# Optimization experiments

Measured on AMD Instinct MI355X. Metric: run time of the kernel, lower is better.

## Reference

```python
import jax, jax.numpy as jnp
import numpy as np

NUM_HEADS = 16
THETA = 10000.0


def _rope(x, pos):
    # x: [B, H, S, d_k], pos: [S] int. Rotate consecutive pairs (even, odd).
    d = x.shape[-1]
    inv_freq = THETA ** (-jnp.arange(0, d, 2, dtype=jnp.float32) / d)  # [d/2]
    ang = pos.astype(jnp.float32)[:, None] * inv_freq                  # [S, d/2]
    cos, sin = jnp.cos(ang), jnp.sin(ang)
    x1, x2 = x[..., 0::2], x[..., 1::2]
    out = jnp.stack([x1 * cos - x2 * sin, x1 * sin + x2 * cos], axis=-1)
    return out.reshape(x.shape)


def setup_inputs() -> dict:
    key = jax.random.key(0)
    k1, k2, k3 = jax.random.split(key, 3)
    B, S, D = 2, 2048, 1024
    x = jax.random.normal(k1, (B, S, D), dtype=jnp.float32)
    # scale weights like a trained init so attention logits are well-behaved
    W_qkv = jax.random.normal(k2, (3 * D, D), dtype=jnp.float32) * 0.02
    W_out = jax.random.normal(k3, (D, D), dtype=jnp.float32) * 0.02
    return {"x": x, "W_qkv": W_qkv, "W_out": W_out}


def reference(x, W_qkv, W_out):
    B, S, D = x.shape
    H = NUM_HEADS
    dk = D // H

    qkv = x @ W_qkv.T                                   # [B, S, 3D]
    q, k, v = jnp.split(qkv, 3, axis=-1)

    def to_heads(t):
        return t.reshape(B, S, H, dk).transpose(0, 2, 1, 3)  # [B, H, S, dk]

    q, k, v = to_heads(q), to_heads(k), to_heads(v)

    pos = jnp.arange(S)
    q = _rope(q, pos)
    k = _rope(k, pos)

    scale = 1.0 / jnp.sqrt(jnp.asarray(dk, dtype=x.dtype))
    logits = jnp.einsum('bhqd,bhkd->bhqk', q, k) * scale  # [B, H, S, S]
    causal = jnp.tril(jnp.ones((S, S), dtype=bool))
    logits = jnp.where(causal, logits, -jnp.inf)
    attn = jax.nn.softmax(logits, axis=-1)
    heads = jnp.einsum('bhqk,bhkd->bhqd', attn, v)        # [B, H, S, dk]
    merged = heads.transpose(0, 2, 1, 3).reshape(B, S, D)
    return merged @ W_out.T
```

## Files before the change

kernel.cpp:

```cpp
#include <hip/hip_runtime.h>
#include <hip/hip_bf16.h>
#include <math.h>

#define BATCH   2
#define SEQ     2048
#define DMODEL  1024
#define NHEAD   16
#define DK      64
#define MTOK    (BATCH*SEQ)
#define QKVN    (3*DMODEL)
#define BH      (BATCH*NHEAD)

typedef __attribute__((ext_vector_type(8))) __bf16 bf16x8;
typedef __attribute__((ext_vector_type(4))) float  f32x4;

#define GL16(gp, lp) __builtin_amdgcn_global_load_lds( \
    (const __attribute__((address_space(1))) unsigned int*)(gp), \
    (__attribute__((address_space(3))) unsigned int*)(lp), 16, 0, 0)

__global__ __launch_bounds__(256) void cvt_bf16(const float* __restrict__ in,
                                                __hip_bfloat16* __restrict__ out, int n) {
    int i = (blockIdx.x * 256 + threadIdx.x) * 4;
    if (i >= n) return;
    float4 v = *(const float4*)(in + i);
    __hip_bfloat162 a, b;
    a.x = __float2bfloat16(v.x); a.y = __float2bfloat16(v.y);
    b.x = __float2bfloat16(v.z); b.y = __float2bfloat16(v.w);
    *(__hip_bfloat162*)(out + i)     = a;
    *(__hip_bfloat162*)(out + i + 2) = b;
}

#define GBM 128
#define GBN 128
#define GBK 32

template<int OUT_BF16>
__global__ __launch_bounds__(256) void gemm_bf16_nt(const __hip_bfloat16* __restrict__ A,
                                                    const __hip_bfloat16* __restrict__ B,
                                                    void* __restrict__ Cv,
                                                    int M, int N, int K) {
    __shared__ __align__(16) __hip_bfloat16 As[GBM][GBK];
    __shared__ __align__(16) __hip_bfloat16 Bs[GBN][GBK];
    const int tid  = threadIdx.x;
    const int wid  = tid >> 6;
    const int lane = tid & 63;
    const int fr   = lane & 15;
    const int fq   = lane >> 4;
    const int wm   = (wid >> 1) * 64;
    const int wn   = (wid & 1) * 64;
    const int m0   = blockIdx.y * GBM;
    const int n0   = blockIdx.x * GBN;

    f32x4 acc[4][4];
#pragma unroll
    for (int m = 0; m < 4; m++)
#pragma unroll
        for (int n = 0; n < 4; n++) acc[m][n] = (f32x4)0.f;

    const __hip_bfloat16* a0 = A + (size_t)(m0 + (tid >> 2)) * K + (tid & 3) * 8;
    const __hip_bfloat16* a1 = a0 + (size_t)64 * K;
    const __hip_bfloat16* b0 = B + (size_t)(n0 + (tid >> 2)) * K + (tid & 3) * 8;
    const __hip_bfloat16* b1 = b0 + (size_t)64 * K;
    __hip_bfloat16* asd0 = &As[0][0] + tid * 8;
    __hip_bfloat16* asd1 = asd0 + 2048;
    __hip_bfloat16* bsd0 = &Bs[0][0] + tid * 8;
    __hip_bfloat16* bsd1 = bsd0 + 2048;

    const __hip_bfloat16* ArP = &As[wm + fr][0] + fq * 8;
    const __hip_bfloat16* BrP = &Bs[wn + fr][0] + fq * 8;

    for (int k0 = 0; k0 < K; k0 += GBK) {
        GL16(a0 + k0, asd0);
        GL16(a1 + k0, asd1);
        GL16(b0 + k0, bsd0);
        GL16(b1 + k0, bsd1);
        __syncthreads();

        bf16x8 af[4], bfv[4];
#pragma unroll
        for (int m = 0; m < 4; m++) af[m]  = *(const bf16x8*)(ArP + m * 512);
#pragma unroll
        for (int n = 0; n < 4; n++) bfv[n] = *(const bf16x8*)(BrP + n * 512);
#pragma unroll
        for (int m = 0; m < 4; m++)
#pragma unroll
            for (int n = 0; n < 4; n++)
                acc[m][n] = __builtin_amdgcn_mfma_f32_16x16x32_bf16(af[m], bfv[n], acc[m][n], 0, 0, 0);
        __syncthreads();
    }

#pragma unroll
    for (int m = 0; m < 4; m++)
#pragma unroll
        for (int n = 0; n < 4; n++)
#pragma unroll
            for (int r = 0; r < 4; r++) {
                size_t row = m0 + wm + m * 16 + fq * 4 + r;
                size_t col = n0 + wn + n * 16 + fr;
                if (OUT_BF16)
                    ((__hip_bfloat16*)Cv)[row * N + col] = __float2bfloat16(acc[m][n][r]);
                else
                    ((float*)Cv)[row * N + col] = acc[m][n][r];
            }
}

__global__ __launch_bounds__(256) void rope_qk(const __hip_bfloat16* __restrict__ qkvb,
                                               __hip_bfloat16* __restrict__ qh,
                                               __hip_bfloat16* __restrict__ kh) {
    int idx  = blockIdx.x * 256 + threadIdx.x;
    int row  = idx >> 10;
    int p    = idx & 1023;
    int half = p >> 9;
    int pp   = p & 511;
    int hh   = pp >> 5;
    int j    = pp & 31;
    int b    = row >> 11, s = row & (SEQ - 1);
    const __hip_bfloat16* src = qkvb + (size_t)row * QKVN + half * DMODEL + hh * DK + 2 * j;
    __hip_bfloat162 xv = *(const __hip_bfloat162*)src;
    float x1 = __bfloat162float(xv.x);
    float x2 = __bfloat162float(xv.y);
    float inv = exp2f(-(float)j * 0.41524101186092030f);
    float ang = (float)s * inv;
    float sn, cs;
    sincosf(ang, &sn, &cs);
    __hip_bfloat162 o;
    o.x = __float2bfloat16(x1 * cs - x2 * sn);
    o.y = __float2bfloat16(x1 * sn + x2 * cs);
    __hip_bfloat16* dst = (half ? kh : qh) + ((size_t)(b * NHEAD + hh) * SEQ + s) * DK + 2 * j;
    *(__hip_bfloat162*)dst = o;
}

__global__ __launch_bounds__(256) void v_trans(const __hip_bfloat16* __restrict__ qkvb,
                                               __hip_bfloat16* __restrict__ vt) {
    const int t  = threadIdx.x;
    const int s  = blockIdx.x * 256 + t;
    const int bh = blockIdx.y;
    const int b  = bh >> 4, h = bh & 15;
    const __hip_bfloat16* src = qkvb + (size_t)(b * SEQ + s) * QKVN + 2 * DMODEL + h * DK;
    __hip_bfloat16* dst = vt + (size_t)bh * DK * SEQ + s;
#pragma unroll
    for (int d2 = 0; d2 < 32; d2++) {
        __hip_bfloat162 v = *(const __hip_bfloat162*)(src + 2 * d2);
        dst[(size_t)(2 * d2) * SEQ]     = v.x;
        dst[(size_t)(2 * d2 + 1) * SEQ] = v.y;
    }
}

__global__ __launch_bounds__(256) void attn_mfma(const __hip_bfloat16* __restrict__ qh,
                                                 const __hip_bfloat16* __restrict__ kh,
                                                 const __hip_bfloat16* __restrict__ vt,
                                                 __hip_bfloat16* __restrict__ mergedb) {
    __shared__ __align__(16) __hip_bfloat16 Ps[4][2048];
    const int tid = threadIdx.x, wid = tid >> 6, lane = tid & 63;
    const int fr = lane & 15, fq = lane >> 4;
    const int bid = blockIdx.x;
    const int qt  = 15 - (bid >> 5);
    const int bh  = bid & 31;
    const int b   = bh >> 4, h = bh & 15;

    const size_t hoff = (size_t)bh * SEQ * DK;
    const __hip_bfloat16* Qb = qh + hoff;
    const __hip_bfloat16* Kb = kh + hoff;
    const __hip_bfloat16* Vb = vt + hoff;

    const int q0 = qt * 128 + wid * 32;

    bf16x8 qf[2][2];
#pragma unroll
    for (int m = 0; m < 2; m++)
#pragma unroll
        for (int c = 0; c < 2; c++)
            qf[m][c] = *(const bf16x8*)&Qb[(size_t)(q0 + m * 16 + fr) * DK + c * 32 + fq * 8];

    f32x4 o[2][4];
#pragma unroll
    for (int m = 0; m < 2; m++)
#pragma unroll
        for (int n = 0; n < 4; n++) o[m][n] = (f32x4)0.f;
    float mrun[8], lrun[8];
#pragma unroll
    for (int i = 0; i < 8; i++) { mrun[i] = -INFINITY; lrun[i] = 0.f; }

    char* Pw = (char*)&Ps[wid][0];
    const int nkt = 2 * qt + 2;

    for (int kt = 0; kt < nkt; kt++) {
        const int key0 = kt * 64;
        f32x4 s_acc[2][4];
#pragma unroll
        for (int m = 0; m < 2; m++)
#pragma unroll
            for (int n = 0; n < 4; n++) s_acc[m][n] = (f32x4)0.f;
#pragma unroll
        for (int n = 0; n < 4; n++) {
            bf16x8 k0f = *(const bf16x8*)&Kb[(size_t)(key0 + n * 16 + fr) * DK + fq * 8];
            bf16x8 k1f = *(const bf16x8*)&Kb[(size_t)(key0 + n * 16 + fr) * DK + 32 + fq * 8];
#pragma unroll
            for (int m = 0; m < 2; m++) {
                s_acc[m][n] = __builtin_amdgcn_mfma_f32_16x16x32_bf16(qf[m][0], k0f, s_acc[m][n], 0, 0, 0);
                s_acc[m][n] = __builtin_amdgcn_mfma_f32_16x16x32_bf16(qf[m][1], k1f, s_acc[m][n], 0, 0, 0);
            }
        }
#pragma unroll
        for (int m = 0; m < 2; m++)
#pragma unroll
            for (int n = 0; n < 4; n++)
#pragma unroll
                for (int r = 0; r < 4; r++) s_acc[m][n][r] *= 0.125f;
        if (kt >= 2 * qt) {
#pragma unroll
            for (int m = 0; m < 2; m++)
#pragma unroll
                for (int n = 0; n < 4; n++)
#pragma unroll
                    for (int r = 0; r < 4; r++) {
                        int qrow = q0 + m * 16 + fq * 4 + r;
                        int key  = key0 + n * 16 + fr;
                        if (key > qrow) s_acc[m][n][r] = -INFINITY;
                    }
        }
#pragma unroll
        for (int m = 0; m < 2; m++)
#pragma unroll
            for (int r = 0; r < 4; r++) {
                float mx = fmaxf(fmaxf(s_acc[m][0][r], s_acc[m][1][r]),
                                 fmaxf(s_acc[m][2][r], s_acc[m][3][r]));
                mx = fmaxf(mx, __shfl_xor(mx, 1));
                mx = fmaxf(mx, __shfl_xor(mx, 2));
                mx = fmaxf(mx, __shfl_xor(mx, 4));
                mx = fmaxf(mx, __shfl_xor(mx, 8));
                const int ri = m * 4 + r;
                float mnew = fmaxf(mrun[ri], mx);
                float corr = __expf(mrun[ri] - mnew);
                mrun[ri] = mnew;
                float rs = 0.f;
#pragma unroll
                for (int n = 0; n < 4; n++) {
                    float pv = __expf(s_acc[m][n][r] - mnew);
                    s_acc[m][n][r] = pv;
                    rs += pv;
                }
                rs += __shfl_xor(rs, 1);
                rs += __shfl_xor(rs, 2);
                rs += __shfl_xor(rs, 4);
                rs += __shfl_xor(rs, 8);
                lrun[ri] = lrun[ri] * corr + rs;
#pragma unroll
                for (int n = 0; n < 4; n++) o[m][n][r] *= corr;
            }
#pragma unroll
        for (int m = 0; m < 2; m++)
#pragma unroll
            for (int r = 0; r < 4; r++) {
                int rl = m * 16 + fq * 4 + r;
                int sw = (rl & 7) << 4;
#pragma unroll
                for (int n = 0; n < 4; n++) {
                    int key = n * 16 + fr;
                    *(__hip_bfloat16*)(Pw + (((rl << 7) + (key << 1)) ^ sw)) =
                        __float2bfloat16(s_acc[m][n][r]);
                }
            }
        asm volatile("s_waitcnt lgkmcnt(0)" ::: "memory");
        __builtin_amdgcn_sched_barrier(0);
        bf16x8 pa[2][2];
#pragma unroll
        for (int m = 0; m < 2; m++)
#pragma unroll
            for (int c = 0; c < 2; c++) {
                int rl = m * 16 + fr;
                pa[m][c] = *(const bf16x8*)(Pw + (((rl << 7) + ((c * 32 + fq * 8) << 1)) ^ ((rl & 7) << 4)));
            }
#pragma unroll
        for (int n = 0; n < 4; n++) {
            bf16x8 v0f = *(const bf16x8*)&Vb[(size_t)(n * 16 + fr) * SEQ + key0 + fq * 8];
            bf16x8 v1f = *(const bf16x8*)&Vb[(size_t)(n * 16 + fr) * SEQ + key0 + 32 + fq * 8];
#pragma unroll
            for (int m = 0; m < 2; m++) {
                o[m][n] = __builtin_amdgcn_mfma_f32_16x16x32_bf16(pa[m][0], v0f, o[m][n], 0, 0, 0);
                o[m][n] = __builtin_amdgcn_mfma_f32_16x16x32_bf16(pa[m][1], v1f, o[m][n], 0, 0, 0);
            }
        }
    }

#pragma unroll
    for (int m = 0; m < 2; m++)
#pragma unroll
        for (int r = 0; r < 4; r++) {
            float invl = 1.0f / lrun[m * 4 + r];
            int qrow = q0 + m * 16 + fq * 4 + r;
#pragma unroll
            for (int n = 0; n < 4; n++) {
                int col = h * DK + n * 16 + fr;
                mergedb[(size_t)(b * SEQ + qrow) * DMODEL + col] =
                    __float2bfloat16(o[m][n][r] * invl);
            }
        }
}

extern "C" void kernel_launch(void* const* d_in, const int* in_sizes, int n_in,
                              void* d_out, int out_size, void* d_ws, size_t ws_size,
                              hipStream_t stream) {
    const float* x    = (const float*)d_in[0];
    const float* Wqkv = (const float*)d_in[1];
    const float* Wout = (const float*)d_in[2];
    float* out = (float*)d_out;

    char* w = (char*)d_ws;
    __hip_bfloat16* qkvb   = (__hip_bfloat16*)(w);
    __hip_bfloat16* qh     = (__hip_bfloat16*)(w + (24u << 20));
    __hip_bfloat16* kh     = (__hip_bfloat16*)(w + (32u << 20));
    __hip_bfloat16* vt     = (__hip_bfloat16*)(w + (40u << 20));
    __hip_bfloat16* xb     = (__hip_bfloat16*)(w + (48u << 20));
    __hip_bfloat16* merged = (__hip_bfloat16*)(w + (48u << 20));
    __hip_bfloat16* wqkvb  = (__hip_bfloat16*)(w + (56u << 20));
    __hip_bfloat16* woutb  = (__hip_bfloat16*)(w + (62u << 20));

    cvt_bf16<<<MTOK * DMODEL / 1024, 256, 0, stream>>>(x, xb, MTOK * DMODEL);
    cvt_bf16<<<QKVN * DMODEL / 1024, 256, 0, stream>>>(Wqkv, wqkvb, QKVN * DMODEL);
    cvt_bf16<<<DMODEL * DMODEL / 1024, 256, 0, stream>>>(Wout, woutb, DMODEL * DMODEL);

    dim3 g1(QKVN / GBN, MTOK / GBM);
    gemm_bf16_nt<1><<<g1, 256, 0, stream>>>(xb, wqkvb, qkvb, MTOK, QKVN, DMODEL);

    rope_qk<<<MTOK * 1024 / 256, 256, 0, stream>>>(qkvb, qh, kh);
    v_trans<<<dim3(SEQ / 256, BH), 256, 0, stream>>>(qkvb, vt);

    attn_mfma<<<512, 256, 0, stream>>>(qh, kh, vt, merged);

    dim3 g3(DMODEL / GBN, MTOK / GBM);
    gemm_bf16_nt<0><<<g3, 256, 0, stream>>>(merged, woutb, out, MTOK, DMODEL, DMODEL);
}
```

Before: 263.0 us.

## Halve attention query tile, double grid, and transpose V through shared memory

```diff
diff --git a/kernel.cpp b/kernel.cpp
--- a/kernel.cpp
+++ b/kernel.cpp
@@ -132,17 +132,29 @@
 
 __global__ __launch_bounds__(256) void v_trans(const __hip_bfloat16* __restrict__ qkvb,
                                                __hip_bfloat16* __restrict__ vt) {
+    __shared__ __hip_bfloat16 Ts[64][72];
     const int t  = threadIdx.x;
-    const int s  = blockIdx.x * 256 + t;
+    const int s0 = blockIdx.x * 64;
     const int bh = blockIdx.y;
     const int b  = bh >> 4, h = bh & 15;
-    const __hip_bfloat16* src = qkvb + (size_t)(b * SEQ + s) * QKVN + 2 * DMODEL + h * DK;
-    __hip_bfloat16* dst = vt + (size_t)bh * DK * SEQ + s;
-#pragma unroll
-    for (int d2 = 0; d2 < 32; d2++) {
-        __hip_bfloat162 v = *(const __hip_bfloat162*)(src + 2 * d2);
-        dst[(size_t)(2 * d2) * SEQ]     = v.x;
-        dst[(size_t)(2 * d2 + 1) * SEQ] = v.y;
+    const int sl = t >> 3;
+    const int dc = (t & 7) * 8;
+#pragma unroll
+    for (int i = 0; i < 2; i++) {
+        int s = sl + i * 32;
+        bf16x8 v = *(const bf16x8*)&qkvb[(size_t)(b * SEQ + s0 + s) * QKVN + 2 * DMODEL + h * DK + dc];
+        *(bf16x8*)&Ts[s][dc] = v;
+    }
+    __syncthreads();
+    const int dl = t >> 3;
+    const int sc = (t & 7) * 8;
+#pragma unroll
+    for (int i = 0; i < 2; i++) {
+        int d = dl + i * 32;
+        bf16x8 o;
+#pragma unroll
+        for (int j = 0; j < 8; j++) o[j] = *(const __bf16*)&Ts[sc + j][d];
+        *(bf16x8*)&vt[(size_t)bh * DK * SEQ + (size_t)d * SEQ + s0 + sc] = o;
     }
 }
 
@@ -150,11 +162,11 @@
                                                  const __hip_bfloat16* __restrict__ kh,
                                                  const __hip_bfloat16* __restrict__ vt,
                                                  __hip_bfloat16* __restrict__ mergedb) {
-    __shared__ __align__(16) __hip_bfloat16 Ps[4][2048];
+    __shared__ __align__(16) __hip_bfloat16 Ps[4][1024];
     const int tid = threadIdx.x, wid = tid >> 6, lane = tid & 63;
     const int fr = lane & 15, fq = lane >> 4;
     const int bid = blockIdx.x;
-    const int qt  = 15 - (bid >> 5);
+    const int qt  = 31 - (bid >> 5);
     const int bh  = bid & 31;
     const int b   = bh >> 4, h = bh & 15;
 
@@ -163,139 +175,124 @@
     const __hip_bfloat16* Kb = kh + hoff;
     const __hip_bfloat16* Vb = vt + hoff;
 
-    const int q0 = qt * 128 + wid * 32;
-
-    bf16x8 qf[2][2];
-#pragma unroll
-    for (int m = 0; m < 2; m++)
-#pragma unroll
-        for (int c = 0; c < 2; c++)
-            qf[m][c] = *(const bf16x8*)&Qb[(size_t)(q0 + m * 16 + fr) * DK + c * 32 + fq * 8];
-
-    f32x4 o[2][4];
-#pragma unroll
-    for (int m = 0; m < 2; m++)
-#pragma unroll
-        for (int n = 0; n < 4; n++) o[m][n] = (f32x4)0.f;
-    float mrun[8], lrun[8];
-#pragma unroll
-    for (int i = 0; i < 8; i++) { mrun[i] = -INFINITY; lrun[i] = 0.f; }
+    const int q0 = qt * 64 + wid * 16;
+
+    bf16x8 qf[2];
+#pragma unroll
+    for (int c = 0; c < 2; c++)
+        qf[c] = *(const bf16x8*)&Qb[(size_t)(q0 + fr) * DK + c * 32 + fq * 8];
+
+    f32x4 o[4];
+#pragma unroll
+    for (int n = 0; n < 4; n++) o[n] = (f32x4)0.f;
+    float mrun[4], lrun[4];
+#pragma unroll
+    for (int i = 0; i < 4; i++) { mrun[i] = -INFINITY; lrun[i] = 0.f; }
 
     char* Pw = (char*)&Ps[wid][0];
-    const int nkt = 2 * qt + 2;
-
-    for (int kt = 0; kt < nkt; kt++) {
+
+    for (int kt = 0; kt <= qt; kt++) {
         const int key0 = kt * 64;
-        f32x4 s_acc[2][4];
-#pragma unroll
-        for (int m = 0; m < 2; m++)
-#pragma unroll
-            for (int n = 0; n < 4; n++) s_acc[m][n] = (f32x4)0.f;
+        bf16x8 kf[4][2];
+#pragma unroll
+        for (int n = 0; n < 4; n++)
+#pragma unroll
+            for (int c = 0; c < 2; c++)
+                kf[n][c] = *(const bf16x8*)&Kb[(size_t)(key0 + n * 16 + fr) * DK + c * 32 + fq * 8];
+        bf16x8 vf[4][2];
+#pragma unroll
+        for (int n = 0; n < 4; n++)
+#pragma unroll
+            for (int c = 0; c < 2; c++)
+                vf[n][c] = *(const bf16x8*)&Vb[(size_t)(n * 16 + fr) * SEQ + key0 + c * 32 + fq * 8];
+
+        f32x4 s_acc[4];
+#pragma unroll
+        for (int n = 0; n < 4; n++) s_acc[n] = (f32x4)0.f;
 #pragma unroll
         for (int n = 0; n < 4; n++) {
-            bf16x8 k0f = *(const bf16x8*)&Kb[(size_t)(key0 + n * 16 + fr) * DK + fq * 8];
-            bf16x8 k1f = *(const bf16x8*)&Kb[(size_t)(key0 + n * 16 + fr) * DK + 32 + fq * 8];
-#pragma unroll
-            for (int m = 0; m < 2; m++) {
-                s_acc[m][n] = __builtin_amdgcn_mfma_f32_16x16x32_bf16(qf[m][0], k0f, s_acc[m][n], 0, 0, 0);
-                s_acc[m][n] = __builtin_amdgcn_mfma_f32_16x16x32_bf16(qf[m][1], k1f, s_acc[m][n], 0, 0, 0);
+            s_acc[n] = __builtin_amdgcn_mfma_f32_16x16x32_bf16(qf[0], kf[n][0], s_acc[n], 0, 0, 0);
+            s_acc[n] = __builtin_amdgcn_mfma_f32_16x16x32_bf16(qf[1], kf[n][1], s_acc[n], 0, 0, 0);
+        }
+#pragma unroll
+        for (int n = 0; n < 4; n++)
+#pragma unroll
+            for (int r = 0; r < 4; r++) s_acc[n][r] *= 0.125f;
+        if (kt == qt) {
+#pragma unroll
+            for (int n = 0; n < 4; n++)
+#pragma unroll
+                for (int r = 0; r < 4; r++) {
+                    int qrow = q0 + fq * 4 + r;
+                    int key  = key0 + n * 16 + fr;
+                    if (key > qrow) s_acc[n][r] = -INFINITY;
+                }
+        }
+
+        float corr[4];
+#pragma unroll
+        for (int r = 0; r < 4; r++) {
+            float mx = fmaxf(fmaxf(s_acc[0][r], s_acc[1][r]),
+                             fmaxf(s_acc[2][r], s_acc[3][r]));
+            mx = fmaxf(mx, __shfl_xor(mx, 1));
+            mx = fmaxf(mx, __shfl_xor(mx, 2));
+            mx = fmaxf(mx, __shfl_xor(mx, 4));
+            mx = fmaxf(mx, __shfl_xor(mx, 8));
+            float mnew = fmaxf(mrun[r], mx);
+            corr[r] = __expf(mrun[r] - mnew);
+            mrun[r] = mnew;
+            float rs = 0.f;
+#pragma unroll
+            for (int n = 0; n < 4; n++) {
+                float pv = __expf(s_acc[n][r] - mnew);
+                s_acc[n][r] = pv;
+                rs += pv;
             }
-        }
-#pragma unroll
-        for (int m = 0; m < 2; m++)
-#pragma unroll
-            for (int n = 0; n < 4; n++)
-#pragma unroll
-                for (int r = 0; r < 4; r++) s_acc[m][n][r] *= 0.125f;
-        if (kt >= 2 * qt) {
-#pragma unroll
-            for (int m = 0; m < 2; m++)
-#pragma unroll
-                for (int n = 0; n < 4; n++)
-#pragma unroll
-                    for (int r = 0; r < 4; r++) {
-                        int qrow = q0 + m * 16 + fq * 4 + r;
-                        int key  = key0 + n * 16 + fr;
-                        if (key > qrow) s_acc[m][n][r] = -INFINITY;
-                    }
-        }
-#pragma unroll
-        for (int m = 0; m < 2; m++)
-#pragma unroll
-            for (int r = 0; r < 4; r++) {
-                float mx = fmaxf(fmaxf(s_acc[m][0][r], s_acc[m][1][r]),
-                                 fmaxf(s_acc[m][2][r], s_acc[m][3][r]));
-                mx = fmaxf(mx, __shfl_xor(mx, 1));
-                mx = fmaxf(mx, __shfl_xor(mx, 2));
-                mx = fmaxf(mx, __shfl_xor(mx, 4));
-                mx = fmaxf(mx, __shfl_xor(mx, 8));
-                const int ri = m * 4 + r;
-                float mnew = fmaxf(mrun[ri], mx);
-                float corr = __expf(mrun[ri] - mnew);
-                mrun[ri] = mnew;
-                float rs = 0.f;
-#pragma unroll
-                for (int n = 0; n < 4; n++) {
-                    float pv = __expf(s_acc[m][n][r] - mnew);
-                    s_acc[m][n][r] = pv;
-                    rs += pv;
-                }
-                rs += __shfl_xor(rs, 1);
-                rs += __shfl_xor(rs, 2);
-                rs += __shfl_xor(rs, 4);
-                rs += __shfl_xor(rs, 8);
-                lrun[ri] = lrun[ri] * corr + rs;
-#pragma unroll
-                for (int n = 0; n < 4; n++) o[m][n][r] *= corr;
+            rs += __shfl_xor(rs, 1);
+            rs += __shfl_xor(rs, 2);
+            rs += __shfl_xor(rs, 4);
+            rs += __shfl_xor(rs, 8);
+            lrun[r] = lrun[r] * corr[r] + rs;
+#pragma unroll
+            for (int n = 0; n < 4; n++) o[n][r] *= corr[r];
+        }
+
+#pragma unroll
+        for (int r = 0; r < 4; r++) {
+            int rl = fq * 4 + r;
+            int sw = (rl & 7) << 4;
+#pragma unroll
+            for (int n = 0; n < 4; n++) {
+                int key = n * 16 + fr;
+                *(__hip_bfloat16*)(Pw + (((rl << 7) + (key << 1)) ^ sw)) =
+                    __float2bfloat16(s_acc[n][r]);
             }
-#pragma unroll
-        for (int m = 0; m < 2; m++)
-#pragma unroll
-            for (int r = 0; r < 4; r++) {
-                int rl = m * 16 + fq * 4 + r;
-                int sw = (rl & 7) << 4;
-#pragma unroll
-                for (int n = 0; n < 4; n++) {
-                    int key = n * 16 + fr;
-                    *(__hip_bfloat16*)(Pw + (((rl << 7) + (key << 1)) ^ sw)) =
-                        __float2bfloat16(s_acc[m][n][r]);
-                }
-            }
+        }
         asm volatile("s_waitcnt lgkmcnt(0)" ::: "memory");
         __builtin_amdgcn_sched_barrier(0);
-        bf16x8 pa[2][2];
-#pragma unroll
-        for (int m = 0; m < 2; m++)
-#pragma unroll
-            for (int c = 0; c < 2; c++) {
-                int rl = m * 16 + fr;
-                pa[m][c] = *(const bf16x8*)(Pw + (((rl << 7) + ((c * 32 + fq * 8) << 1)) ^ ((rl & 7) << 4)));
-            }
+
+        bf16x8 pa[2];
+#pragma unroll
+        for (int c = 0; c < 2; c++)
+            pa[c] = *(const bf16x8*)(Pw + (((fr << 7) + ((c * 32 + fq * 8) << 1)) ^ ((fr & 7) << 4)));
 #pragma unroll
         for (int n = 0; n < 4; n++) {
-            bf16x8 v0f = *(const bf16x8*)&Vb[(size_t)(n * 16 + fr) * SEQ + key0 + fq * 8];
-            bf16x8 v1f = *(const bf16x8*)&Vb[(size_t)(n * 16 + fr) * SEQ + key0 + 32 + fq * 8];
-#pragma unroll
-            for (int m = 0; m < 2; m++) {
-                o[m][n] = __builtin_amdgcn_mfma_f32_16x16x32_bf16(pa[m][0], v0f, o[m][n], 0, 0, 0);
-                o[m][n] = __builtin_amdgcn_mfma_f32_16x16x32_bf16(pa[m][1], v1f, o[m][n], 0, 0, 0);
-            }
-        }
-    }
-
-#pragma unroll
-    for (int m = 0; m < 2; m++)
-#pragma unroll
-        for (int r = 0; r < 4; r++) {
-            float invl = 1.0f / lrun[m * 4 + r];
-            int qrow = q0 + m * 16 + fq * 4 + r;
-#pragma unroll
-            for (int n = 0; n < 4; n++) {
-                int col = h * DK + n * 16 + fr;
-                mergedb[(size_t)(b * SEQ + qrow) * DMODEL + col] =
-                    __float2bfloat16(o[m][n][r] * invl);
-            }
-        }
+            o[n] = __builtin_amdgcn_mfma_f32_16x16x32_bf16(pa[0], vf[n][0], o[n], 0, 0, 0);
+            o[n] = __builtin_amdgcn_mfma_f32_16x16x32_bf16(pa[1], vf[n][1], o[n], 0, 0, 0);
+        }
+    }
+
+#pragma unroll
+    for (int r = 0; r < 4; r++) {
+        float invl = 1.0f / lrun[r];
+        int qrow = q0 + fq * 4 + r;
+#pragma unroll
+        for (int n = 0; n < 4; n++) {
+            int col = h * DK + n * 16 + fr;
+            mergedb[(size_t)(b * SEQ + qrow) * DMODEL + col] =
+                __float2bfloat16(o[n][r] * invl);
+        }
+    }
 }
 
 extern "C" void kernel_launch(void* const* d_in, const int* in_sizes, int n_in,
@@ -324,9 +321,9 @@
     gemm_bf16_nt<1><<<g1, 256, 0, stream>>>(xb, wqkvb, qkvb, MTOK, QKVN, DMODEL);
 
     rope_qk<<<MTOK * 1024 / 256, 256, 0, stream>>>(qkvb, qh, kh);
-    v_trans<<<dim3(SEQ / 256, BH), 256, 0, stream>>>(qkvb, vt);
-
-    attn_mfma<<<512, 256, 0, stream>>>(qh, kh, vt, merged);
+    v_trans<<<dim3(SEQ / 64, BH), 256, 0, stream>>>(qkvb, vt);
+
+    attn_mfma<<<1024, 256, 0, stream>>>(qh, kh, vt, merged);
 
     dim3 g3(DMODEL / GBN, MTOK / GBM);
     gemm_bf16_nt<0><<<g3, 256, 0, stream>>>(merged, woutb, out, MTOK, DMODEL, DMODEL);
```

Result: slower. 291.7 us (+10.9%).

## Stage K/V tiles through double-buffered LDS with async loads in attention

Applied to the files above, without the earlier changes.

```diff
diff --git a/kernel.cpp b/kernel.cpp
--- a/kernel.cpp
+++ b/kernel.cpp
@@ -123,26 +123,39 @@
     float ang = (float)s * inv;
     float sn, cs;
     sincosf(ang, &sn, &cs);
+    float sc = half ? 1.0f : 0.125f;
     __hip_bfloat162 o;
-    o.x = __float2bfloat16(x1 * cs - x2 * sn);
-    o.y = __float2bfloat16(x1 * sn + x2 * cs);
+    o.x = __float2bfloat16((x1 * cs - x2 * sn) * sc);
+    o.y = __float2bfloat16((x1 * sn + x2 * cs) * sc);
     __hip_bfloat16* dst = (half ? kh : qh) + ((size_t)(b * NHEAD + hh) * SEQ + s) * DK + 2 * j;
     *(__hip_bfloat162*)dst = o;
 }
 
 __global__ __launch_bounds__(256) void v_trans(const __hip_bfloat16* __restrict__ qkvb,
                                                __hip_bfloat16* __restrict__ vt) {
+    __shared__ __hip_bfloat16 Ts[64][72];
     const int t  = threadIdx.x;
-    const int s  = blockIdx.x * 256 + t;
+    const int s0 = blockIdx.x * 64;
     const int bh = blockIdx.y;
     const int b  = bh >> 4, h = bh & 15;
-    const __hip_bfloat16* src = qkvb + (size_t)(b * SEQ + s) * QKVN + 2 * DMODEL + h * DK;
-    __hip_bfloat16* dst = vt + (size_t)bh * DK * SEQ + s;
-#pragma unroll
-    for (int d2 = 0; d2 < 32; d2++) {
-        __hip_bfloat162 v = *(const __hip_bfloat162*)(src + 2 * d2);
-        dst[(size_t)(2 * d2) * SEQ]     = v.x;
-        dst[(size_t)(2 * d2 + 1) * SEQ] = v.y;
+    const int sl = t >> 3;
+    const int dc = (t & 7) * 8;
+#pragma unroll
+    for (int i = 0; i < 2; i++) {
+        int s = sl + i * 32;
+        bf16x8 v = *(const bf16x8*)&qkvb[(size_t)(b * SEQ + s0 + s) * QKVN + 2 * DMODEL + h * DK + dc];
+        *(bf16x8*)&Ts[s][dc] = v;
+    }
+    __syncthreads();
+    const int dl = t >> 3;
+    const int sc = (t & 7) * 8;
+#pragma unroll
+    for (int i = 0; i < 2; i++) {
+        int d = dl + i * 32;
+        bf16x8 o;
+#pragma unroll
+        for (int j = 0; j < 8; j++) o[j] = *(const __bf16*)&Ts[sc + j][d];
+        *(bf16x8*)&vt[(size_t)bh * DK * SEQ + (size_t)d * SEQ + s0 + sc] = o;
     }
 }
 
@@ -150,6 +163,8 @@
                                                  const __hip_bfloat16* __restrict__ kh,
                                                  const __hip_bfloat16* __restrict__ vt,
                                                  __hip_bfloat16* __restrict__ mergedb) {
+    __shared__ __align__(16) __hip_bfloat16 Kbuf[2][4096];
+    __shared__ __align__(16) __hip_bfloat16 Vbuf[2][4096];
     __shared__ __align__(16) __hip_bfloat16 Ps[4][2048];
     const int tid = threadIdx.x, wid = tid >> 6, lane = tid & 63;
     const int fr = lane & 15, fq = lane >> 4;
@@ -160,10 +175,29 @@
 
     const size_t hoff = (size_t)bh * SEQ * DK;
     const __hip_bfloat16* Qb = qh + hoff;
-    const __hip_bfloat16* Kb = kh + hoff;
-    const __hip_bfloat16* Vb = vt + hoff;
-
-    const int q0 = qt * 128 + wid * 32;
+    const char* Kc = (const char*)(kh + hoff);
+    const char* Vc = (const char*)(vt + hoff);
+
+    const int q0  = qt * 128 + wid * 32;
+    const int nkt = 2 * qt + 2;
+
+    const int L0 = tid * 16, L1 = L0 + 4096;
+    const int r0 = L0 >> 7,  r1 = L1 >> 7;
+    const int ks0 = L0 ^ ((r0 & 7) << 4);
+    const int ks1 = L1 ^ ((r1 & 7) << 4);
+    const int vc0 = (L0 & 127) ^ ((r0 & 7) << 4);
+    const int vc1 = (L1 & 127) ^ ((r1 & 7) << 4);
+
+    auto stage = [&](int kts) {
+        const char* Kt = Kc + (size_t)kts * 8192;
+        const char* Vt = Vc + (size_t)kts * 128;
+        char* kd = (char*)&Kbuf[kts & 1][0];
+        char* vd = (char*)&Vbuf[kts & 1][0];
+        GL16(Kt + ks0, kd + L0);
+        GL16(Kt + ks1, kd + L1);
+        GL16(Vt + (size_t)r0 * 4096 + vc0, vd + L0);
+        GL16(Vt + (size_t)r1 * 4096 + vc1, vd + L1);
+    };
 
     bf16x8 qf[2][2];
 #pragma unroll
@@ -182,105 +216,125 @@
     for (int i = 0; i < 8; i++) { mrun[i] = -INFINITY; lrun[i] = 0.f; }
 
     char* Pw = (char*)&Ps[wid][0];
-    const int nkt = 2 * qt + 2;
+    const int swf = (fr & 7) << 4;
+
+    stage(0);
+    __syncthreads();
 
     for (int kt = 0; kt < nkt; kt++) {
+        if (kt + 1 < nkt) stage(kt + 1);
         const int key0 = kt * 64;
-        f32x4 s_acc[2][4];
-#pragma unroll
-        for (int m = 0; m < 2; m++)
-#pragma unroll
-            for (int n = 0; n < 4; n++) s_acc[m][n] = (f32x4)0.f;
-#pragma unroll
-        for (int n = 0; n < 4; n++) {
-            bf16x8 k0f = *(const bf16x8*)&Kb[(size_t)(key0 + n * 16 + fr) * DK + fq * 8];
-            bf16x8 k1f = *(const bf16x8*)&Kb[(size_t)(key0 + n * 16 + fr) * DK + 32 + fq * 8];
-#pragma unroll
-            for (int m = 0; m < 2; m++) {
-                s_acc[m][n] = __builtin_amdgcn_mfma_f32_16x16x32_bf16(qf[m][0], k0f, s_acc[m][n], 0, 0, 0);
-                s_acc[m][n] = __builtin_amdgcn_mfma_f32_16x16x32_bf16(qf[m][1], k1f, s_acc[m][n], 0, 0, 0);
+        const bool active = (key0 <= q0 + 31);
+        if (active) {
+            const char* Kl = (const char*)&Kbuf[kt & 1][0];
+            const char* Vl = (const char*)&Vbuf[kt & 1][0];
+            bf16x8 kf[4][2];
+#pragma unroll
+            for (int n = 0; n < 4; n++)
+#pragma unroll
+                for (int c = 0; c < 2; c++)
+                    kf[n][c] = *(const bf16x8*)(Kl + ((((n * 16 + fr) << 7) + (c << 6) + (fq << 4)) ^ swf));
+
+            f32x4 s_acc[2][4];
+#pragma unroll
+            for (int m = 0; m < 2; m++)
+#pragma unroll
+                for (int n = 0; n < 4; n++) s_acc[m][n] = (f32x4)0.f;
+            __builtin_amdgcn_s_setprio(1);
+#pragma unroll
+            for (int n = 0; n < 4; n++)
+#pragma unroll
+                for (int m = 0; m < 2; m++) {
+                    s_acc[m][n] = __builtin_amdgcn_mfma_f32_16x16x32_bf16(qf[m][0], kf[n][0], s_acc[m][n], 0, 0, 0);
+                    s_acc[m][n] = __builtin_amdgcn_mfma_f32_16x16x32_bf16(qf[m][1], kf[n][1], s_acc[m][n], 0, 0, 0);
+                }
+            __builtin_amdgcn_s_setprio(0);
+
+            if (key0 + 63 > q0) {
+#pragma unroll
+                for (int m = 0; m < 2; m++)
+#pragma unroll
+                    for (int n = 0; n < 4; n++)
+#pragma unroll
+                        for (int r = 0; r < 4; r++) {
+                            int qrow = q0 + m * 16 + fq * 4 + r;
+                            int key  = key0 + n * 16 + fr;
+                            if (key > qrow) s_acc[m][n][r] = -INFINITY;
+                        }
             }
+
+#pragma unroll
+            for (int m = 0; m < 2; m++)
+#pragma unroll
+                for (int r = 0; r < 4; r++) {
+                    float mx = fmaxf(fmaxf(s_acc[m][0][r], s_acc[m][1][r]),
+                                     fmaxf(s_acc[m][2][r], s_acc[m][3][r]));
+                    mx = fmaxf(mx, __shfl_xor(mx, 1));
+                    mx = fmaxf(mx, __shfl_xor(mx, 2));
+                    mx = fmaxf(mx, __shfl_xor(mx, 4));
+                    mx = fmaxf(mx, __shfl_xor(mx, 8));
+                    const int ri = m * 4 + r;
+                    float mnew = fmaxf(mrun[ri], mx);
+                    float corr = __expf(mrun[ri] - mnew);
+                    mrun[ri] = mnew;
+                    float rs = 0.f;
+#pragma unroll
+                    for (int n = 0; n < 4; n++) {
+                        float pv = __expf(s_acc[m][n][r] - mnew);
+                        s_acc[m][n][r] = pv;
+                        rs += pv;
+                    }
+                    rs += __shfl_xor(rs, 1);
+                    rs += __shfl_xor(rs, 2);
+                    rs += __shfl_xor(rs, 4);
+                    rs += __shfl_xor(rs, 8);
+                    lrun[ri] = lrun[ri] * corr + rs;
+#pragma unroll
+                    for (int n = 0; n < 4; n++) o[m][n][r] *= corr;
+                }
+
+            bf16x8 vf[4][2];
+#pragma unroll
+            for (int n = 0; n < 4; n++)
+#pragma unroll
+                for (int c = 0; c < 2; c++)
+                    vf[n][c] = *(const bf16x8*)(Vl + ((((n * 16 + fr) << 7) + (c << 6) + (fq << 4)) ^ swf));
+
+#pragma unroll
+            for (int m = 0; m < 2; m++)
+#pragma unroll
+                for (int r = 0; r < 4; r++) {
+                    int rl = m * 16 + fq * 4 + r;
+                    int sw = (rl & 7) << 4;
+#pragma unroll
+                    for (int n = 0; n < 4; n++) {
+                        int key = n * 16 + fr;
+                        *(__hip_bfloat16*)(Pw + (((rl << 7) + (key << 1)) ^ sw)) =
+                            __float2bfloat16(s_acc[m][n][r]);
+                    }
+                }
+            asm volatile("s_waitcnt lgkmcnt(0)" ::: "memory");
+            __builtin_amdgcn_sched_barrier(0);
+
+            bf16x8 pa[2][2];
+#pragma unroll
+            for (int m = 0; m < 2; m++)
+#pragma unroll
+                for (int c = 0; c < 2; c++) {
+                    int rl = m * 16 + fr;
+                    pa[m][c] = *(const bf16x8*)(Pw + (((rl << 7) + ((c * 32 + fq * 8) << 1)) ^ ((rl & 7) << 4)));
+                }
+            __builtin_amdgcn_s_setprio(1);
+#pragma unroll
+            for (int n = 0; n < 4; n++)
+#pragma unroll
+                for (int m = 0; m < 2; m++) {
+                    o[m][n] = __builtin_amdgcn_mfma_f32_16x16x32_bf16(pa[m][0], vf[n][0], o[m][n], 0, 0, 0);
+                    o[m][n] = __builtin_amdgcn_mfma_f32_16x16x32_bf16(pa[m][1], vf[n][1], o[m][n], 0, 0, 0);
+                }
+            __builtin_amdgcn_s_setprio(0);
         }
-#pragma unroll
-        for (int m = 0; m < 2; m++)
-#pragma unroll
-            for (int n = 0; n < 4; n++)
-#pragma unroll
-                for (int r = 0; r < 4; r++) s_acc[m][n][r] *= 0.125f;
-        if (kt >= 2 * qt) {
-#pragma unroll
-            for (int m = 0; m < 2; m++)
-#pragma unroll
-                for (int n = 0; n < 4; n++)
-#pragma unroll
-                    for (int r = 0; r < 4; r++) {
-                        int qrow = q0 + m * 16 + fq * 4 + r;
-                        int key  = key0 + n * 16 + fr;
-                        if (key > qrow) s_acc[m][n][r] = -INFINITY;
-                    }
-        }
-#pragma unroll
-        for (int m = 0; m < 2; m++)
-#pragma unroll
-            for (int r = 0; r < 4; r++) {
-                float mx = fmaxf(fmaxf(s_acc[m][0][r], s_acc[m][1][r]),
-                                 fmaxf(s_acc[m][2][r], s_acc[m][3][r]));
-                mx = fmaxf(mx, __shfl_xor(mx, 1));
-                mx = fmaxf(mx, __shfl_xor(mx, 2));
-                mx = fmaxf(mx, __shfl_xor(mx, 4));
-                mx = fmaxf(mx, __shfl_xor(mx, 8));
-                const int ri = m * 4 + r;
-                float mnew = fmaxf(mrun[ri], mx);
-                float corr = __expf(mrun[ri] - mnew);
-                mrun[ri] = mnew;
-                float rs = 0.f;
-#pragma unroll
-                for (int n = 0; n < 4; n++) {
-                    float pv = __expf(s_acc[m][n][r] - mnew);
-                    s_acc[m][n][r] = pv;
-                    rs += pv;
-                }
-                rs += __shfl_xor(rs, 1);
-                rs += __shfl_xor(rs, 2);
-                rs += __shfl_xor(rs, 4);
-                rs += __shfl_xor(rs, 8);
-                lrun[ri] = lrun[ri] * corr + rs;
-#pragma unroll
-                for (int n = 0; n < 4; n++) o[m][n][r] *= corr;
-            }
-#pragma unroll
-        for (int m = 0; m < 2; m++)
-#pragma unroll
-            for (int r = 0; r < 4; r++) {
-                int rl = m * 16 + fq * 4 + r;
-                int sw = (rl & 7) << 4;
-#pragma unroll
-                for (int n = 0; n < 4; n++) {
-                    int key = n * 16 + fr;
-                    *(__hip_bfloat16*)(Pw + (((rl << 7) + (key << 1)) ^ sw)) =
-                        __float2bfloat16(s_acc[m][n][r]);
-                }
-            }
-        asm volatile("s_waitcnt lgkmcnt(0)" ::: "memory");
-        __builtin_amdgcn_sched_barrier(0);
-        bf16x8 pa[2][2];
-#pragma unroll
-        for (int m = 0; m < 2; m++)
-#pragma unroll
-            for (int c = 0; c < 2; c++) {
-                int rl = m * 16 + fr;
-                pa[m][c] = *(const bf16x8*)(Pw + (((rl << 7) + ((c * 32 + fq * 8) << 1)) ^ ((rl & 7) << 4)));
-            }
-#pragma unroll
-        for (int n = 0; n < 4; n++) {
-            bf16x8 v0f = *(const bf16x8*)&Vb[(size_t)(n * 16 + fr) * SEQ + key0 + fq * 8];
-            bf16x8 v1f = *(const bf16x8*)&Vb[(size_t)(n * 16 + fr) * SEQ + key0 + 32 + fq * 8];
-#pragma unroll
-            for (int m = 0; m < 2; m++) {
-                o[m][n] = __builtin_amdgcn_mfma_f32_16x16x32_bf16(pa[m][0], v0f, o[m][n], 0, 0, 0);
-                o[m][n] = __builtin_amdgcn_mfma_f32_16x16x32_bf16(pa[m][1], v1f, o[m][n], 0, 0, 0);
-            }
-        }
+        __syncthreads();
     }
 
 #pragma unroll
@@ -324,7 +378,7 @@
     gemm_bf16_nt<1><<<g1, 256, 0, stream>>>(xb, wqkvb, qkvb, MTOK, QKVN, DMODEL);
 
     rope_qk<<<MTOK * 1024 / 256, 256, 0, stream>>>(qkvb, qh, kh);
-    v_trans<<<dim3(SEQ / 256, BH), 256, 0, stream>>>(qkvb, vt);
+    v_trans<<<dim3(SEQ / 64, BH), 256, 0, stream>>>(qkvb, vt);
 
     attn_mfma<<<512, 256, 0, stream>>>(qh, kh, vt, merged);
 
```

Result: no change. 258.5 us (-1.7%).
